# Performance work log

Measured on AMD Instinct MI355X. Metric: run time of the kernel, lower is better.

Reference implementation:

```python
import jax, jax.numpy as jnp
import numpy as np

B, T, C, H = 1, 2048, 1024, 16
K = C // H


def _ln(x, g, b):
    m = x.mean(-1, keepdims=True)
    v = ((x - m) ** 2).mean(-1, keepdims=True)
    return (x - m) * jax.lax.rsqrt(v + 1e-5) * g + b


def setup_inputs() -> dict:
    key = jax.random.key(0)
    ks = jax.random.split(key, 16)
    n = lambda k, s, sc=1.0: jax.random.normal(k, s, jnp.float32) * sc
    u = lambda k, s: jax.random.uniform(k, s, jnp.float32)
    ws = C ** -0.5
    return {
        "x": n(ks[0], (B, T, C)),
        "shift_state": n(ks[1], (B, C)),
        "time_maa_x": u(ks[2], (1, 1, C)),
        "time_maa_r": u(ks[3], (1, 1, C)),
        "time_maa_k": u(ks[4], (1, 1, C)),
        "time_maa_v": u(ks[5], (1, 1, C)),
        "time_maa_w1": n(ks[6], (C, 96), 0.01),
        "time_maa_w2": n(ks[7], (3, 32, C), 0.01),
        "headavg_w1": n(ks[8], (C, 4 * 2 * H), 0.01),
        "headavg_w2": n(ks[9], (4, 2 * H, H), 0.01),
        "w_r": n(ks[10], (C, C), ws),
        "w_k": n(ks[11], (C, C), ws),
        "w_v": n(ks[12], (C, C), ws),
        "w_o": n(ks[13], (C, C), ws),
        "ln_r_g": jnp.ones((C,)), "ln_r_b": jnp.zeros((C,)),
        "ln_k_g": jnp.ones((C,)), "ln_k_b": jnp.zeros((C,)),
        "ln_v_g": jnp.ones((C,)), "ln_v_b": jnp.zeros((C,)),
        "ln_x_g": jnp.ones((C,)), "ln_x_b": jnp.zeros((C,)),
    }


def reference(x, shift_state, time_maa_x, time_maa_r, time_maa_k, time_maa_v,
              time_maa_w1, time_maa_w2, headavg_w1, headavg_w2,
              w_r, w_k, w_v, w_o,
              ln_r_g, ln_r_b, ln_k_g, ln_k_b, ln_v_g, ln_v_b, ln_x_g, ln_x_b):
    Bs, Ts, Cs = x.shape
    Hh = headavg_w2.shape[-1]
    Kk = Cs // Hh

    # token shift
    dxprev = jnp.concatenate([shift_state[:, None, :], x[:, :-1]], axis=1) - x

    # LoRA token-shift mixing
    xxx = jnp.tanh((x + dxprev * time_maa_x) @ time_maa_w1)       # [B,T,3*32]
    mix = jnp.einsum('btnd,ndc->nbtc', xxx.reshape(Bs, Ts, 3, -1), time_maa_w2)
    mq, mk, mv = mix[0], mix[1], mix[2]
    xq = x + dxprev * (time_maa_r + mq)
    xk = x + dxprev * (time_maa_k + mk)
    xv = x + dxprev * (time_maa_v + mv)

    q = _ln(xq @ w_r, ln_r_g, ln_r_b).reshape(Bs, Ts, Hh, Kk).transpose(0, 2, 1, 3)
    k = _ln(xk @ w_k, ln_k_g, ln_k_b).reshape(Bs, Ts, Hh, Kk).transpose(0, 2, 1, 3)
    v = _ln(xv @ w_v, ln_v_g, ln_v_b).reshape(Bs, Ts, Hh, Kk).transpose(0, 2, 1, 3)

    # per-head LoRA score mixing coefficients
    ha = jnp.tanh(x @ headavg_w1).reshape(Bs, Ts, 4, -1)          # [B,T,4,2H]
    hm = jnp.einsum('btnd,ndh->nbth', ha, headavg_w2) / Hh        # [4,B,T,H]
    pre_q, pre_k, post_q, post_k = hm[0], hm[1], hm[2], hm[3]

    scale = Kk ** -0.5
    y = jnp.einsum('bhtk,bhsk->bhts', q * scale, k)               # [B,H,T,S]
    y = y + jnp.einsum('bhts,bth->bts', y, pre_q)[:, None]
    y = y + jnp.einsum('bhts,bsh->bts', y, pre_k)[:, None]

    # causal ALiBi bias
    rel = (jnp.arange(Ts)[:, None] - jnp.arange(Ts)[None, :]).astype(x.dtype)
    slopes = (2.0 ** (-8.0 * jnp.arange(1, Hh + 1, dtype=x.dtype) / Hh))
    bias = jnp.where(rel >= 0, -slopes[:, None, None] * rel, jnp.asarray(-1e9, x.dtype))
    y = y + bias[None]

    y = jax.nn.softmax(y, axis=-1)
    y = y + jnp.einsum('bhts,bth->bts', y, post_q)[:, None]
    y = y + jnp.einsum('bhts,bsh->bts', y, post_k)[:, None]

    out = jnp.einsum('bhts,bhsv->bhtv', y, v).transpose(0, 2, 1, 3).reshape(Bs, Ts, Cs)
    out = _ln(out, ln_x_g, ln_x_b) @ w_o
    return out
```

## Files before the change

### kernel.cpp

```cpp
#include <hip/hip_runtime.h>
#include <cstdint>
#include <cstddef>


#define C_DIM 1024
#define HEADS 16
#define TQ 16
#define SCH 256
#define PADS 40
#define EPS 36

typedef unsigned short ushort_t;
typedef __attribute__((ext_vector_type(8))) short bf16x8;
typedef __attribute__((ext_vector_type(4))) float f32x4;

#define MFMA16(a, b, c) __builtin_amdgcn_mfma_f32_16x16x32_bf16(a, b, c, 0, 0, 0)

__device__ __forceinline__ unsigned int f2bf_u(float f) {
  unsigned int u = __float_as_uint(f);
  return (u + 0x7fffu + ((u >> 16) & 1u)) >> 16;
}
__device__ __forceinline__ float bf2f(ushort_t u) {
  return __uint_as_float(((unsigned int)u) << 16);
}
__device__ __forceinline__ void pack4(ushort_t* dst, float x0, float x1,
                                      float x2, float x3) {
  uint2 v;
  v.x = f2bf_u(x0) | (f2bf_u(x1) << 16);
  v.y = f2bf_u(x2) | (f2bf_u(x3) << 16);
  *(uint2*)dst = v;
}
__device__ __forceinline__ void mlmerge(float& M, float& L, float m2, float l2) {
  float nm = fmaxf(M, m2);
  float ea = (M  <= -1e29f) ? 0.f : __expf(M - nm);
  float eb = (m2 <= -1e29f) ? 0.f : __expf(m2 - nm);
  L = L * ea + l2 * eb;
  M = nm;
}

#define EPHASE(HQARR, HKARR, SSUM) do {                                      \
  if (tid < 128) {                                                           \
    const int tcq = tid >> 3, sq = tid & 7;                                  \
    const int sob = (s1 - sbeg) + sq*4;                                      \
    float a4[4] = {0.f,0.f,0.f,0.f}, b4[4] = {0.f,0.f,0.f,0.f};              \
    _Pragma("unroll")                                                        \
    for (int hq4 = 0; hq4 < 4; hq4++) {                                      \
      float hqa[4];                                                          \
      *(float4*)hqa = *(const float4*)&HQARR[tcq*16 + hq4*4];                \
      float hka[4][4];                                                       \
      _Pragma("unroll")                                                      \
      for (int c = 0; c < 4; c++)                                            \
        *(float4*)hka[c] = *(const float4*)&HKARR[(sob + c)*16 + hq4*4];     \
      _Pragma("unroll")                                                      \
      for (int j = 0; j < 4; j++) {                                          \
        const uint2 yr = *(const uint2*)                                     \
            &ybuf[((hq4*4 + j)*TQ + tcq)*PADS + sq*4];                       \
        float yv[4];                                                         \
        yv[0] = bf2f((ushort_t)(yr.x & 0xffffu));                            \
        yv[1] = bf2f((ushort_t)(yr.x >> 16));                                \
        yv[2] = bf2f((ushort_t)(yr.y & 0xffffu));                            \
        yv[3] = bf2f((ushort_t)(yr.y >> 16));                                \
        _Pragma("unroll")                                                    \
        for (int c = 0; c < 4; c++) {                                        \
          a4[c] += yv[c] * hqa[j];                                           \
          b4[c] += yv[c] * hka[c][j];                                        \
        }                                                                    \
      }                                                                      \
    }                                                                        \
    float ssum[4];                                                           \
    *(float4*)ssum = *(const float4*)&SSUM[sob];                             \
    float4 eo;                                                               \
    eo.x = a4[0]*(1.f + ssum[0]) + b4[0];                                    \
    eo.y = a4[1]*(1.f + ssum[1]) + b4[1];                                    \
    eo.z = a4[2]*(1.f + ssum[2]) + b4[2];                                    \
    eo.w = a4[3]*(1.f + ssum[3]) + b4[3];                                    \
    *(float4*)&ep[tcq*EPS + sq*4] = eo;                                      \
  }                                                                          \
} while (0)

__global__ __launch_bounds__(256) void prep_kernel(
    const float* __restrict__ x, const float* __restrict__ shift,
    const float* __restrict__ maa_x,
    float* __restrict__ dxprev, ushort_t* __restrict__ zbf,
    ushort_t* __restrict__ xbf)
{
  const int t = blockIdx.x;
  const int c = threadIdx.x * 4;
  const size_t base = (size_t)t * C_DIM + c;
  const float4 xc = *(const float4*)&x[base];
  const float4 xp = (t == 0) ? *(const float4*)&shift[c]
                             : *(const float4*)&x[base - C_DIM];
  const float4 mx = *(const float4*)&maa_x[c];
  float4 d;
  d.x = xp.x - xc.x; d.y = xp.y - xc.y; d.z = xp.z - xc.z; d.w = xp.w - xc.w;
  *(float4*)&dxprev[base] = d;
  pack4(&zbf[base], xc.x + d.x*mx.x, xc.y + d.y*mx.y,
        xc.z + d.z*mx.z, xc.w + d.w*mx.w);
  pack4(&xbf[base], xc.x, xc.y, xc.z, xc.w);
}

__global__ __launch_bounds__(256) void wlora_prep(
    const float* __restrict__ w1, const float* __restrict__ hw1,
    ushort_t* __restrict__ wlt)
{
  __shared__ float tile[32][33];
  const int k0 = blockIdx.x*32, j0 = blockIdx.y*32;
  const int r = threadIdx.x >> 3, c4 = (threadIdx.x & 7) * 4;
  const float* W = (j0 < 96) ? w1 : hw1;
  const int stride = (j0 < 96) ? 96 : 128;
  const int jo = (j0 < 96) ? j0 : j0 - 96;
  const float4 v = *(const float4*)&W[(size_t)(k0+r)*stride + jo + c4];
  tile[r][c4+0] = v.x; tile[r][c4+1] = v.y;
  tile[r][c4+2] = v.z; tile[r][c4+3] = v.w;
  __syncthreads();
  pack4(&wlt[(size_t)(j0+r)*C_DIM + k0 + c4],
        tile[c4+0][r], tile[c4+1][r], tile[c4+2][r], tile[c4+3][r]);
}

__global__ __launch_bounds__(64)
__attribute__((amdgpu_waves_per_eu(2, 4)))
void lora_gemm(
    const ushort_t* __restrict__ zbf, const ushort_t* __restrict__ xbf,
    const ushort_t* __restrict__ wlt, float* __restrict__ xxx,
    float* __restrict__ ha)
{
  const int nt = blockIdx.y;
  const int bm = blockIdx.x * 32;
  const ushort_t* A = (nt < 3) ? zbf : xbf;
  const int wrow = nt * 32;
  const int lane = threadIdx.x;
  const int l15 = lane & 15, g = lane >> 4;
  f32x4 acc[2][2];
  #pragma unroll
  for (int i = 0; i < 2; i++)
    #pragma unroll
    for (int j = 0; j < 2; j++) acc[i][j] = (f32x4){0.f,0.f,0.f,0.f};
  bf16x8 a0[2], b0[2], a1[2], b1[2];
  #define LLA(dst, kk) { \
    dst[0] = *(const bf16x8*)&A[(size_t)(bm + l15)*C_DIM + (kk) + g*8]; \
    dst[1] = *(const bf16x8*)&A[(size_t)(bm + 16 + l15)*C_DIM + (kk) + g*8]; }
  #define LLB(dst, kk) { \
    dst[0] = *(const bf16x8*)&wlt[(size_t)(wrow + l15)*C_DIM + (kk) + g*8]; \
    dst[1] = *(const bf16x8*)&wlt[(size_t)(wrow + 16 + l15)*C_DIM + (kk) + g*8]; }
  LLA(a0, 0); LLB(b0, 0);
  for (int k0 = 0; k0 < C_DIM; k0 += 64) {
    LLA(a1, k0+32); LLB(b1, k0+32);
    #pragma unroll
    for (int i = 0; i < 2; i++)
      #pragma unroll
      for (int j = 0; j < 2; j++) acc[i][j] = MFMA16(a0[i], b0[j], acc[i][j]);
    if (k0 + 64 < C_DIM) { LLA(a0, k0+64); LLB(b0, k0+64); }
    #pragma unroll
    for (int i = 0; i < 2; i++)
      #pragma unroll
      for (int j = 0; j < 2; j++) acc[i][j] = MFMA16(a1[i], b1[j], acc[i][j]);
  }
  #undef LLA
  #undef LLB
  #pragma unroll
  for (int i = 0; i < 2; i++)
    #pragma unroll
    for (int j = 0; j < 2; j++)
      #pragma unroll
      for (int r = 0; r < 4; r++) {
        const int t = bm + i*16 + g*4 + r;
        const int col = wrow + j*16 + l15;
        const float val = tanhf(acc[i][j][r]);
        if (nt < 3) xxx[(size_t)t*96 + col] = val;
        else        ha[(size_t)t*128 + col - 96] = val;
      }
}

__global__ __launch_bounds__(256) void mix_kernel(
    const float* __restrict__ x, const float* __restrict__ dxp,
    const float* __restrict__ xxx,
    const float* __restrict__ maa_r, const float* __restrict__ maa_k,
    const float* __restrict__ maa_v, const float* __restrict__ w2,
    ushort_t* __restrict__ xq, ushort_t* __restrict__ xk,
    ushort_t* __restrict__ xv)
{
  __shared__ float xs[8][96];
  const int t0 = blockIdx.x * 8;
  const int tid = threadIdx.x;
  #pragma unroll
  for (int i = 0; i < 3; i++) {
    const int u = tid + i*256;
    if (u < 768) {
      const int r = u / 96, cc = u % 96;
      xs[r][cc] = xxx[(size_t)(t0+r)*96 + cc];
    }
  }
  __syncthreads();
  const int c = tid * 4;
  float4 xc[8], dx[8];
  #pragma unroll
  for (int r = 0; r < 8; r++) {
    xc[r] = *(const float4*)&x[(size_t)(t0+r)*C_DIM + c];
    dx[r] = *(const float4*)&dxp[(size_t)(t0+r)*C_DIM + c];
  }
  const float* maas[3] = {maa_r, maa_k, maa_v};
  ushort_t* outs[3] = {xq, xk, xv};
  #pragma unroll
  for (int n = 0; n < 3; n++) {
    const float4 mv = *(const float4*)&maas[n][c];
    float m[8][4];
    #pragma unroll
    for (int r = 0; r < 8; r++) {
      m[r][0] = mv.x; m[r][1] = mv.y; m[r][2] = mv.z; m[r][3] = mv.w;
    }
    #pragma unroll 8
    for (int d = 0; d < 32; d++) {
      const float4 w = *(const float4*)&w2[((size_t)n*32 + d)*C_DIM + c];
      #pragma unroll
      for (int r = 0; r < 8; r++) {
        const float xv2 = xs[r][n*32 + d];
        m[r][0] += xv2*w.x; m[r][1] += xv2*w.y;
        m[r][2] += xv2*w.z; m[r][3] += xv2*w.w;
      }
    }
    #pragma unroll
    for (int r = 0; r < 8; r++)
      pack4(&outs[n][(size_t)(t0+r)*C_DIM + c],
            xc[r].x + dx[r].x*m[r][0], xc[r].y + dx[r].y*m[r][1],
            xc[r].z + dx[r].z*m[r][2], xc[r].w + dx[r].w*m[r][3]);
  }
}

__global__ __launch_bounds__(256) void hm_kernel(
    const float* __restrict__ ha, const float* __restrict__ hw2,
    float* __restrict__ hm, int T)
{
  const int t = blockIdx.x*4 + (threadIdx.x >> 6);
  const int u = threadIdx.x & 63;
  const int n = u >> 4, h = u & 15;
  float s = 0.f;
  #pragma unroll 8
  for (int d = 0; d < 32; d++)
    s += ha[(size_t)t*128 + n*32 + d] * hw2[(size_t)(n*32 + d)*16 + h];
  hm[((size_t)n*T + t)*16 + h] = s * (1.f/16.f);
}

__global__ __launch_bounds__(256) void wprep_kernel(
    const float* __restrict__ w0, const float* __restrict__ w1,
    const float* __restrict__ w2, const float* __restrict__ w3,
    ushort_t* __restrict__ o0, ushort_t* __restrict__ o1,
    ushort_t* __restrict__ o2, ushort_t* __restrict__ o3)
{
  const float* W; ushort_t* O;
  if (blockIdx.z == 0)      { W = w0; O = o0; }
  else if (blockIdx.z == 1) { W = w1; O = o1; }
  else if (blockIdx.z == 2) { W = w2; O = o2; }
  else                      { W = w3; O = o3; }
  __shared__ float tile[32][33];
  const int k0 = blockIdx.x*32, n0 = blockIdx.y*32;
  const int r = threadIdx.x >> 3, c4 = (threadIdx.x & 7) * 4;
  const float4 v = *(const float4*)&W[(size_t)(k0+r)*C_DIM + n0 + c4];
  tile[r][c4+0] = v.x; tile[r][c4+1] = v.y;
  tile[r][c4+2] = v.z; tile[r][c4+3] = v.w;
  __syncthreads();
  pack4(&O[(size_t)(n0+r)*C_DIM + k0 + c4],
        tile[c4+0][r], tile[c4+1][r], tile[c4+2][r], tile[c4+3][r]);
}

__global__ __launch_bounds__(64)
__attribute__((amdgpu_waves_per_eu(2, 4)))
void gemm_bf16(
    const ushort_t* __restrict__ A, const ushort_t* __restrict__ Bt,
    float* __restrict__ Cm)
{
  const int bid = blockIdx.x;
  const int bn = (bid & 15) * 64;
  const int bm = (bid >> 4) * 32;
  const int lane = threadIdx.x;
  const int l15 = lane & 15, g = lane >> 4;
  f32x4 acc[2][4];
  #pragma unroll
  for (int i = 0; i < 2; i++)
    #pragma unroll
    for (int j = 0; j < 4; j++) acc[i][j] = (f32x4){0.f,0.f,0.f,0.f};
  bf16x8 a0[2], b0[4], a1[2], b1[4];
  #define LGA(dst, kk) { \
    _Pragma("unroll") \
    for (int i = 0; i < 2; i++) \
      dst[i] = *(const bf16x8*)&A[(size_t)(bm + i*16 + l15)*C_DIM + (kk) + g*8]; }
  #define LGB(dst, kk) { \
    _Pragma("unroll") \
    for (int j = 0; j < 4; j++) \
      dst[j] = *(const bf16x8*)&Bt[(size_t)(bn + j*16 + l15)*C_DIM + (kk) + g*8]; }
  LGA(a0, 0); LGB(b0, 0);
  for (int k0 = 0; k0 < C_DIM; k0 += 64) {
    LGA(a1, k0+32); LGB(b1, k0+32);
    #pragma unroll
    for (int i = 0; i < 2; i++)
      #pragma unroll
      for (int j = 0; j < 4; j++) acc[i][j] = MFMA16(a0[i], b0[j], acc[i][j]);
    if (k0 + 64 < C_DIM) { LGA(a0, k0+64); LGB(b0, k0+64); }
    #pragma unroll
    for (int i = 0; i < 2; i++)
      #pragma unroll
      for (int j = 0; j < 4; j++) acc[i][j] = MFMA16(a1[i], b1[j], acc[i][j]);
  }
  #undef LGA
  #undef LGB
  #pragma unroll
  for (int i = 0; i < 2; i++)
    #pragma unroll
    for (int j = 0; j < 4; j++)
      #pragma unroll
      for (int r = 0; r < 4; r++)
        Cm[(size_t)(bm + i*16 + g*4 + r)*C_DIM + bn + j*16 + l15] = acc[i][j][r];
}

__global__ __launch_bounds__(256) void ln_rows(
    const float* __restrict__ in, ushort_t* __restrict__ outp,
    const float* __restrict__ g, const float* __restrict__ b, float scale)
{
  __shared__ float red[4];
  const int t = blockIdx.x;
  const int tid = threadIdx.x;
  const int c = tid*4;
  const float4 v = *(const float4*)&in[(size_t)t*C_DIM + c];
  float s = v.x+v.y+v.z+v.w;
  #pragma unroll
  for (int off = 32; off > 0; off >>= 1) s += __shfl_down(s, off, 64);
  if ((tid & 63) == 0) red[tid >> 6] = s;
  __syncthreads();
  const float mean = (red[0]+red[1]+red[2]+red[3]) * (1.0f/C_DIM);
  __syncthreads();
  const float d0 = v.x-mean, d1 = v.y-mean, d2 = v.z-mean, d3 = v.w-mean;
  float q = d0*d0 + d1*d1 + d2*d2 + d3*d3;
  #pragma unroll
  for (int off = 32; off > 0; off >>= 1) q += __shfl_down(q, off, 64);
  if ((tid & 63) == 0) red[tid >> 6] = q;
  __syncthreads();
  const float var = (red[0]+red[1]+red[2]+red[3]) * (1.0f/C_DIM);
  const float rstd = rsqrtf(var + 1e-5f);
  const float4 gv = *(const float4*)&g[c];
  const float4 bv = *(const float4*)&b[c];
  pack4(outp + (size_t)t*C_DIM + c,
        (d0*rstd*gv.x + bv.x)*scale, (d1*rstd*gv.y + bv.y)*scale,
        (d2*rstd*gv.z + bv.z)*scale, (d3*rstd*gv.w + bv.w)*scale);
}

__global__ __launch_bounds__(256) void vtrans_kernel(
    const ushort_t* __restrict__ vbf, ushort_t* __restrict__ Vt, int T)
{
  __shared__ ushort_t tile[32][36];
  const int t0 = blockIdx.x*32, c0 = blockIdx.y*32;
  const int r = threadIdx.x >> 3, c4 = (threadIdx.x & 7) * 4;
  const uint2 raw = *(const uint2*)&vbf[(size_t)(t0+r)*C_DIM + c0 + c4];
  tile[r][c4+0] = (ushort_t)(raw.x & 0xffffu);
  tile[r][c4+1] = (ushort_t)(raw.x >> 16);
  tile[r][c4+2] = (ushort_t)(raw.y & 0xffffu);
  tile[r][c4+3] = (ushort_t)(raw.y >> 16);
  __syncthreads();
  uint2 w;
  w.x = (unsigned)tile[c4+0][r] | ((unsigned)tile[c4+1][r] << 16);
  w.y = (unsigned)tile[c4+2][r] | ((unsigned)tile[c4+3][r] << 16);
  *(uint2*)&Vt[(size_t)(c0+r)*T + t0 + c4] = w;
}

__global__ __launch_bounds__(512)
__attribute__((amdgpu_waves_per_eu(2, 4)))
void attn_stats(
    const ushort_t* __restrict__ qbf, const ushort_t* __restrict__ kbf,
    const float* __restrict__ hmb, float* __restrict__ part_m,
    float* __restrict__ part_l, int T)
{
  __shared__ ushort_t ybuf[HEADS*TQ*PADS];
  __shared__ float ep[TQ*EPS];
  __shared__ float hpqf[TQ*16];
  __shared__ float hpkf[SCH*16];
  __shared__ float spk_l[SCH];

  const int tbi = (int)blockIdx.y;
  const int tb = (T/TQ) - 1 - tbi;
  const int sc = (tbi & 1) ? (7 - (int)blockIdx.x) : (int)blockIdx.x;
  const int t0 = tb * TQ;
  const int sbeg = sc * SCH;
  if (sbeg >= t0 + TQ) return;
  const int send = (sbeg + SCH < t0 + TQ) ? (sbeg + SCH) : (t0 + TQ);

  const int tid = threadIdx.x;
  const int w = tid >> 6, lane = tid & 63, l15 = lane & 15, g = lane >> 4;

  for (int i = tid; i < SCH*16; i += 512)
    hpkf[i] = hmb[((size_t)1*T + sbeg)*16 + i];
  if (tid < TQ*16)
    hpqf[tid] = hmb[((size_t)0*T + t0)*16 + tid];
  if (tid < SCH) {
    const float* src = hmb + ((size_t)1*T + sbeg + tid)*16;
    float s = 0.f;
    #pragma unroll
    for (int q4 = 0; q4 < 4; q4++) {
      const float4 v = *(const float4*)&src[q4*4];
      s += v.x + v.y + v.z + v.w;
    }
    spk_l[tid] = s;
  }

  const int hh[2] = {w, w + 8};
  bf16x8 qf[2][2];
  float slope[2];
  #pragma unroll
  for (int hd = 0; hd < 2; hd++) {
    #pragma unroll
    for (int kc = 0; kc < 2; kc++)
      qf[hd][kc] = *(const bf16x8*)
          &qbf[(size_t)(t0 + l15)*C_DIM + hh[hd]*64 + kc*32 + g*8];
    slope[hd] = exp2f(-0.5f * (float)(hh[hd] + 1));
  }
  float mrun[2] = {-1e30f, -1e30f}, lrun[2] = {0.f, 0.f};

  bf16x8 kf[2][2][2];
  #define LOADK(sbase) { \
    _Pragma("unroll") \
    for (int hd = 0; hd < 2; hd++) \
      _Pragma("unroll") \
      for (int sh = 0; sh < 2; sh++) \
        _Pragma("unroll") \
        for (int kc = 0; kc < 2; kc++) \
          kf[hd][sh][kc] = *(const bf16x8*)&kbf[ \
              (size_t)((sbase) + sh*16 + l15)*C_DIM + hh[hd]*64 + kc*32 + g*8]; }
  LOADK(sbeg);

  for (int s1 = sbeg; s1 < send; s1 += 32) {
    f32x4 acc[2][2];
    #pragma unroll
    for (int hd = 0; hd < 2; hd++)
      #pragma unroll
      for (int sh = 0; sh < 2; sh++) acc[hd][sh] = (f32x4){0.f,0.f,0.f,0.f};
    #pragma unroll
    for (int hd = 0; hd < 2; hd++) {
      #pragma unroll
      for (int sh = 0; sh < 2; sh++)
        #pragma unroll
        for (int kc = 0; kc < 2; kc++)
          acc[hd][sh] = MFMA16(kf[hd][sh][kc], qf[hd][kc], acc[hd][sh]);
      #pragma unroll
      for (int sh = 0; sh < 2; sh++)
        pack4(&ybuf[(size_t)(hh[hd]*TQ + l15)*PADS + sh*16 + g*4],
              acc[hd][sh][0], acc[hd][sh][1], acc[hd][sh][2], acc[hd][sh][3]);
    }
    {
      const int snx = (s1 + 32 < send) ? s1 + 32 : s1;
      LOADK(snx);
    }
    __syncthreads();
    EPHASE(hpqf, hpkf, spk_l);
    __syncthreads();
    float epv[2][4];
    #pragma unroll
    for (int sh = 0; sh < 2; sh++)
      *(float4*)epv[sh] = *(const float4*)&ep[l15*EPS + sh*16 + g*4];
    #pragma unroll
    for (int hd = 0; hd < 2; hd++) {
      const int t = t0 + l15;
      #pragma unroll
      for (int sh = 0; sh < 2; sh++)
        #pragma unroll
        for (int r = 0; r < 4; r++) {
          const int s = s1 + sh*16 + g*4 + r;
          if (s <= t) {
            const float y3 = acc[hd][sh][r] + epv[sh][r]
                - slope[hd]*(float)(t - s);
            const float d = y3 - mrun[hd];
            if (d > 0.f) { lrun[hd] = lrun[hd]*__expf(-d) + 1.f; mrun[hd] = y3; }
            else lrun[hd] += __expf(d);
          }
        }
    }
  }
  #undef LOADK
  #pragma unroll
  for (int hd = 0; hd < 2; hd++) {
    float M = mrun[hd], L = lrun[hd];
    #pragma unroll
    for (int mask = 16; mask < 64; mask <<= 1) {
      const float M2 = __shfl_xor(M, mask, 64);
      const float L2 = __shfl_xor(L, mask, 64);
      mlmerge(M, L, M2, L2);
    }
    if (g == 0) {
      part_m[(size_t)(sc*HEADS + hh[hd])*T + t0 + l15] = M;
      part_l[(size_t)(sc*HEADS + hh[hd])*T + t0 + l15] = L;
    }
  }
}

__global__ __launch_bounds__(256) void ml_combine(
    const float* __restrict__ part_m, const float* __restrict__ part_l,
    float* __restrict__ m_fin, float* __restrict__ linv, int T)
{
  const int idx = blockIdx.x*256 + threadIdx.x;
  const int t = idx & (T - 1);
  const int nsc = (t >> 8) + 1;
  float M = -1e30f, L = 0.f;
  for (int sc = 0; sc < nsc; sc++)
    mlmerge(M, L, part_m[(size_t)sc*HEADS*T + idx],
            part_l[(size_t)sc*HEADS*T + idx]);
  m_fin[idx] = M;
  linv[idx] = 1.f / L;
}

__global__ __launch_bounds__(512)
__attribute__((amdgpu_waves_per_eu(2, 4)))
void attn_apply(
    const ushort_t* __restrict__ qbf, const ushort_t* __restrict__ kbf,
    const ushort_t* __restrict__ Vt, const float* __restrict__ hmb,
    const float* __restrict__ m_fin, const float* __restrict__ linv,
    float* __restrict__ P, int T)
{
  __shared__ ushort_t ybuf[HEADS*TQ*PADS];
  __shared__ float ep[TQ*EPS];
  __shared__ float hpqf[TQ*16], hoqf[TQ*16];
  __shared__ float hpkf[SCH*16], hokf[SCH*16];
  __shared__ float spk_l[SCH], spo_l[SCH];

  const int tbi = (int)blockIdx.y;
  const int tb = (T/TQ) - 1 - tbi;
  const int sc = (tbi & 1) ? (7 - (int)blockIdx.x) : (int)blockIdx.x;
  const int t0 = tb * TQ;
  const int sbeg = sc * SCH;
  if (sbeg >= t0 + TQ) return;
  const int send = (sbeg + SCH < t0 + TQ) ? (sbeg + SCH) : (t0 + TQ);
  const int prow0 = T*sc - 128*sc*(sc-1) - SCH*sc;

  const int tid = threadIdx.x;
  const int w = tid >> 6, lane = tid & 63, l15 = lane & 15, g = lane >> 4;

  for (int i = tid; i < SCH*16; i += 512) {
    hpkf[i] = hmb[((size_t)1*T + sbeg)*16 + i];
    hokf[i] = hmb[((size_t)3*T + sbeg)*16 + i];
  }
  if (tid < TQ*16) {
    hpqf[tid] = hmb[((size_t)0*T + t0)*16 + tid];
    hoqf[tid] = hmb[((size_t)2*T + t0)*16 + tid];
  }
  {
    const int s_l = tid & 255;
    const float* src = hmb + ((size_t)((tid < 256) ? 1 : 3)*T + sbeg + s_l)*16;
    float s = 0.f;
    #pragma unroll
    for (int q4 = 0; q4 < 4; q4++) {
      const float4 v = *(const float4*)&src[q4*4];
      s += v.x + v.y + v.z + v.w;
    }
    if (tid < 256) spk_l[s_l] = s; else spo_l[s_l] = s;
  }

  const int hh[2] = {w, w + 8};
  bf16x8 qf[2][2];
  float mt[2], li[2], slope[2];
  #pragma unroll
  for (int hd = 0; hd < 2; hd++) {
    #pragma unroll
    for (int kc = 0; kc < 2; kc++)
      qf[hd][kc] = *(const bf16x8*)
          &qbf[(size_t)(t0 + l15)*C_DIM + hh[hd]*64 + kc*32 + g*8];
    mt[hd] = m_fin[(size_t)hh[hd]*T + t0 + l15];
    li[hd] = linv[(size_t)hh[hd]*T + t0 + l15];
    slope[hd] = exp2f(-0.5f * (float)(hh[hd] + 1));
  }
  f32x4 oacc[2][4];
  #pragma unroll
  for (int hd = 0; hd < 2; hd++)
    #pragma unroll
    for (int vf = 0; vf < 4; vf++) oacc[hd][vf] = (f32x4){0.f,0.f,0.f,0.f};

  for (int s1 = sbeg; s1 < send; s1 += 32) {
    f32x4 acc[2][2];
    #pragma unroll
    for (int hd = 0; hd < 2; hd++)
      #pragma unroll
      for (int sh = 0; sh < 2; sh++) acc[hd][sh] = (f32x4){0.f,0.f,0.f,0.f};
    #pragma unroll
    for (int hd = 0; hd < 2; hd++) {
      #pragma unroll
      for (int sh = 0; sh < 2; sh++)
        #pragma unroll
        for (int kc = 0; kc < 2; kc++) {
          const bf16x8 kf = *(const bf16x8*)
              &kbf[(size_t)(s1 + sh*16 + l15)*C_DIM + hh[hd]*64 + kc*32 + g*8];
          acc[hd][sh] = MFMA16(kf, qf[hd][kc], acc[hd][sh]);
        }
      #pragma unroll
      for (int sh = 0; sh < 2; sh++)
        pack4(&ybuf[(size_t)(hh[hd]*TQ + l15)*PADS + sh*16 + g*4],
              acc[hd][sh][0], acc[hd][sh][1], acc[hd][sh][2], acc[hd][sh][3]);
    }
    __syncthreads();
    EPHASE(hpqf, hpkf, spk_l);
    __syncthreads();
    {
      float epv[2][4];
      #pragma unroll
      for (int sh = 0; sh < 2; sh++)
        *(float4*)epv[sh] = *(const float4*)&ep[l15*EPS + sh*16 + g*4];
      #pragma unroll
      for (int hd = 0; hd < 2; hd++) {
        const int t = t0 + l15;
        #pragma unroll
        for (int sh = 0; sh < 2; sh++) {
          #pragma unroll
          for (int r = 0; r < 4; r++) {
            const int s = s1 + sh*16 + g*4 + r;
            float p = 0.f;
            if (s <= t) {
              const float y3 = acc[hd][sh][r] + epv[sh][r]
                  - slope[hd]*(float)(t - s);
              p = __expf(y3 - mt[hd]) * li[hd];
            }
            acc[hd][sh][r] = p;
          }
          pack4(&ybuf[(size_t)(hh[hd]*TQ + l15)*PADS + sh*16 + g*4],
                acc[hd][sh][0], acc[hd][sh][1], acc[hd][sh][2], acc[hd][sh][3]);
        }
      }
    }
    __syncthreads();
    EPHASE(hoqf, hokf, spo_l);
    __syncthreads();
    bf16x8 vv[2][4];
    #pragma unroll
    for (int hd = 0; hd < 2; hd++)
      #pragma unroll
      for (int vf = 0; vf < 4; vf++)
        vv[hd][vf] = *(const bf16x8*)
            &Vt[(size_t)(hh[hd]*64 + vf*16 + l15)*T + s1 + g*8];
    {
      float epv[2][4];
      #pragma unroll
      for (int sh = 0; sh < 2; sh++)
        *(float4*)epv[sh] = *(const float4*)&ep[l15*EPS + sh*16 + g*4];
      #pragma unroll
      for (int hd = 0; hd < 2; hd++)
        #pragma unroll
        for (int sh = 0; sh < 2; sh++)
          pack4(&ybuf[(size_t)(hh[hd]*TQ + l15)*PADS + sh*16 + g*4],
                acc[hd][sh][0] + epv[sh][0], acc[hd][sh][1] + epv[sh][1],
                acc[hd][sh][2] + epv[sh][2], acc[hd][sh][3] + epv[sh][3]);
    }
    #pragma unroll
    for (int hd = 0; hd < 2; hd++) {
      const bf16x8 pa = *(const bf16x8*)
          &ybuf[(size_t)(hh[hd]*TQ + l15)*PADS + g*8];
      #pragma unroll
      for (int vf = 0; vf < 4; vf++)
        oacc[hd][vf] = MFMA16(pa, vv[hd][vf], oacc[hd][vf]);
    }
  }
  #pragma unroll
  for (int hd = 0; hd < 2; hd++)
    #pragma unroll
    for (int vf = 0; vf < 4; vf++)
      #pragma unroll
      for (int r = 0; r < 4; r++)
        P[(size_t)(prow0 + t0 + g*4 + r)*C_DIM + hh[hd]*64 + vf*16 + l15]
            = oacc[hd][vf][r];
}

__global__ __launch_bounds__(256) void reduce_ln(
    const float* __restrict__ P, ushort_t* __restrict__ outp,
    const float* __restrict__ g, const float* __restrict__ b, int T)
{
  __shared__ float red[4];
  const int t = blockIdx.x;
  const int tid = threadIdx.x;
  const int c = tid*4;
  const int nsc = (t >> 8) + 1;
  float4 v = make_float4(0.f, 0.f, 0.f, 0.f);
  int off = 0;
  for (int sc = 0; sc < nsc; sc++) {
    const int row = off + t - sc*SCH;
    const float4 pv = *(const float4*)&P[(size_t)row*C_DIM + c];
    v.x += pv.x; v.y += pv.y; v.z += pv.z; v.w += pv.w;
    off += T - SCH*sc;
  }
  float s = v.x+v.y+v.z+v.w;
  #pragma unroll
  for (int o = 32; o > 0; o >>= 1) s += __shfl_down(s, o, 64);
  if ((tid & 63) == 0) red[tid >> 6] = s;
  __syncthreads();
  const float mean = (red[0]+red[1]+red[2]+red[3]) * (1.0f/C_DIM);
  __syncthreads();
  const float d0 = v.x-mean, d1 = v.y-mean, d2 = v.z-mean, d3 = v.w-mean;
  float q = d0*d0 + d1*d1 + d2*d2 + d3*d3;
  #pragma unroll
  for (int o = 32; o > 0; o >>= 1) q += __shfl_down(q, o, 64);
  if ((tid & 63) == 0) red[tid >> 6] = q;
  __syncthreads();
  const float var = (red[0]+red[1]+red[2]+red[3]) * (1.0f/C_DIM);
  const float rstd = rsqrtf(var + 1e-5f);
  const float4 gv = *(const float4*)&g[c];
  const float4 bv = *(const float4*)&b[c];
  pack4(outp + (size_t)t*C_DIM + c,
        d0*rstd*gv.x + bv.x, d1*rstd*gv.y + bv.y,
        d2*rstd*gv.z + bv.z, d3*rstd*gv.w + bv.w);
}

extern "C" void kernel_launch(void* const* d_in, const int* in_sizes, int n_in,
                              void* d_out, int out_size, void* d_ws, size_t ws_size,
                              hipStream_t stream)
{
  const float* x      = (const float*)d_in[0];
  const float* shift  = (const float*)d_in[1];
  const float* maa_x  = (const float*)d_in[2];
  const float* maa_r  = (const float*)d_in[3];
  const float* maa_k  = (const float*)d_in[4];
  const float* maa_v  = (const float*)d_in[5];
  const float* w1     = (const float*)d_in[6];
  const float* w2     = (const float*)d_in[7];
  const float* hw1    = (const float*)d_in[8];
  const float* hw2    = (const float*)d_in[9];
  const float* w_r    = (const float*)d_in[10];
  const float* w_k    = (const float*)d_in[11];
  const float* w_v    = (const float*)d_in[12];
  const float* w_o    = (const float*)d_in[13];
  const float* ln_r_g = (const float*)d_in[14];
  const float* ln_r_b = (const float*)d_in[15];
  const float* ln_k_g = (const float*)d_in[16];
  const float* ln_k_b = (const float*)d_in[17];
  const float* ln_v_g = (const float*)d_in[18];
  const float* ln_v_b = (const float*)d_in[19];
  const float* ln_x_g = (const float*)d_in[20];
  const float* ln_x_b = (const float*)d_in[21];

  const int T = in_sizes[0] / C_DIM;
  const size_t MM = (size_t)T * C_DIM;
  const size_t HF = MM / 2;

  float* ws = (float*)d_ws;
  float*    P      = ws;
  float*    dxprev = ws;
  ushort_t* zbf    = (ushort_t*)(ws + MM);
  ushort_t* xbf    = (ushort_t*)(ws + MM + HF);
  float*    gtmp   = ws + 2*MM;
  ushort_t* xqb    = (ushort_t*)(ws + 3*MM);
  ushort_t* xkb    = (ushort_t*)(ws + 3*MM + HF);
  ushort_t* xvb    = (ushort_t*)(ws + 4*MM);
  float* base2 = ws + 4*MM + HF;
  ushort_t* qbf = (ushort_t*)(base2 + 0*HF);
  ushort_t* kbf = (ushort_t*)(base2 + 1*HF);
  ushort_t* vbf = (ushort_t*)(base2 + 2*HF);
  ushort_t* Vt  = (ushort_t*)(base2 + 3*HF);
  ushort_t* wtr = (ushort_t*)(base2 + 4*HF);
  ushort_t* wtk = wtr + (size_t)C_DIM*C_DIM;
  ushort_t* wtv = wtk + (size_t)C_DIM*C_DIM;
  ushort_t* wto = wtv + (size_t)C_DIM*C_DIM;
  float* after_w = base2 + 4*HF + (size_t)2*C_DIM*C_DIM;
  ushort_t* wlt = (ushort_t*)after_w;
  float* xxx    = after_w + 131072;
  float* ha     = xxx + (size_t)T*96;
  float* hmb    = ha + (size_t)T*128;
  float* part_m = hmb + (size_t)4*T*16;
  float* part_l = part_m + (size_t)8*HEADS*T;
  float* m_fin  = part_l + (size_t)8*HEADS*T;
  float* linv   = m_fin + (size_t)HEADS*T;
  ushort_t* abf = (ushort_t*)(linv + (size_t)HEADS*T);

  prep_kernel<<<T, 256, 0, stream>>>(x, shift, maa_x, dxprev, zbf, xbf);
  wlora_prep<<<dim3(C_DIM/32, 7), 256, 0, stream>>>(w1, hw1, wlt);
  lora_gemm<<<dim3(T/32, 7), 64, 0, stream>>>(zbf, xbf, wlt, xxx, ha);
  mix_kernel<<<T/8, 256, 0, stream>>>(x, dxprev, xxx, maa_r, maa_k, maa_v, w2,
                                      xqb, xkb, xvb);
  hm_kernel<<<T/4, 256, 0, stream>>>(ha, hw2, hmb, T);
  wprep_kernel<<<dim3(32, 32, 4), 256, 0, stream>>>(
      w_r, w_k, w_v, w_o, wtr, wtk, wtv, wto);

  const int ggemm = (T/32) * (C_DIM/64);
  gemm_bf16<<<ggemm, 64, 0, stream>>>(xqb, wtr, gtmp);
  ln_rows<<<T, 256, 0, stream>>>(gtmp, qbf, ln_r_g, ln_r_b, 0.125f);
  gemm_bf16<<<ggemm, 64, 0, stream>>>(xkb, wtk, gtmp);
  ln_rows<<<T, 256, 0, stream>>>(gtmp, kbf, ln_k_g, ln_k_b, 1.0f);
  gemm_bf16<<<ggemm, 64, 0, stream>>>(xvb, wtv, gtmp);
  ln_rows<<<T, 256, 0, stream>>>(gtmp, vbf, ln_v_g, ln_v_b, 1.0f);
  vtrans_kernel<<<dim3(T/32, C_DIM/32), 256, 0, stream>>>(vbf, Vt, T);

  attn_stats<<<dim3(8, T/TQ), 512, 0, stream>>>(
      qbf, kbf, hmb, part_m, part_l, T);
  ml_combine<<<(HEADS*T)/256, 256, 0, stream>>>(part_m, part_l, m_fin, linv, T);
  attn_apply<<<dim3(8, T/TQ), 512, 0, stream>>>(
      qbf, kbf, Vt, hmb, m_fin, linv, P, T);

  reduce_ln<<<T, 256, 0, stream>>>(P, abf, ln_x_g, ln_x_b, T);
  gemm_bf16<<<ggemm, 64, 0, stream>>>(abf, wto, (float*)d_out);
}
```

Measured before the change: 545.4 us.

## Precompute pre-softmax head-mixing term as a single extended-K GEMM

Folds the pre_q/pre_k cross-head mixing of raw scores into one dense T×T matrix E. E is computed by a new bf16 MFMA GEMM over concatenated [q*pre_q, q] and [k*(1+sum pre_k), k*pre_k] operands. The stats and apply attention kernels then read E from global memory instead of rebuilding it per tile through LDS with two barriers per step. This removes the per-tile EPHASE pass and its synchronisation, at the cost of an extra T×T fp32 buffer write and read, a prep kernel, and bf16 rounding of the scaled operands.

```diff
diff --git a/kernel.cpp b/kernel.cpp
--- a/kernel.cpp
+++ b/kernel.cpp
@@ -360,19 +360,95 @@
   *(uint2*)&Vt[(size_t)(c0+r)*T + t0 + c4] = w;
 }
 
+__global__ __launch_bounds__(256) void qek_prep(
+    const ushort_t* __restrict__ qbf, const ushort_t* __restrict__ kbf,
+    const float* __restrict__ hmb, ushort_t* __restrict__ Qe,
+    ushort_t* __restrict__ Ke, int T)
+{
+  const int t = blockIdx.x;
+  const int tid = threadIdx.x;
+  const int c4 = tid * 4;
+  const int h = tid >> 4;
+  float sp = 0.f;
+  #pragma unroll
+  for (int q4 = 0; q4 < 4; q4++) {
+    const float4 v = *(const float4*)&hmb[((size_t)1*T + t)*16 + q4*4];
+    sp += v.x + v.y + v.z + v.w;
+  }
+  const float preq = hmb[((size_t)0*T + t)*16 + h];
+  const float prek = hmb[((size_t)1*T + t)*16 + h];
+  const uint2 qr = *(const uint2*)&qbf[(size_t)t*C_DIM + c4];
+  const uint2 kr = *(const uint2*)&kbf[(size_t)t*C_DIM + c4];
+  float qv[4], kv[4];
+  qv[0] = bf2f((ushort_t)(qr.x & 0xffffu)); qv[1] = bf2f((ushort_t)(qr.x >> 16));
+  qv[2] = bf2f((ushort_t)(qr.y & 0xffffu)); qv[3] = bf2f((ushort_t)(qr.y >> 16));
+  kv[0] = bf2f((ushort_t)(kr.x & 0xffffu)); kv[1] = bf2f((ushort_t)(kr.x >> 16));
+  kv[2] = bf2f((ushort_t)(kr.y & 0xffffu)); kv[3] = bf2f((ushort_t)(kr.y >> 16));
+  const size_t rb = (size_t)t * 2048;
+  pack4(&Qe[rb + c4], qv[0]*preq, qv[1]*preq, qv[2]*preq, qv[3]*preq);
+  *(uint2*)&Qe[rb + 1024 + c4] = qr;
+  const float osp = 1.f + sp;
+  pack4(&Ke[rb + c4], kv[0]*osp, kv[1]*osp, kv[2]*osp, kv[3]*osp);
+  pack4(&Ke[rb + 1024 + c4], kv[0]*prek, kv[1]*prek, kv[2]*prek, kv[3]*prek);
+}
+
+__global__ __launch_bounds__(64)
+__attribute__((amdgpu_waves_per_eu(2, 4)))
+void e_gemm(
+    const ushort_t* __restrict__ Qe, const ushort_t* __restrict__ Ke,
+    float* __restrict__ E, int T)
+{
+  const int bm = blockIdx.y * 32;
+  const int bn = blockIdx.x * 64;
+  if (bn > bm + 31) return;
+  const int lane = threadIdx.x;
+  const int l15 = lane & 15, g = lane >> 4;
+  const int KD = 2048;
+  f32x4 acc[2][4];
+  #pragma unroll
+  for (int i = 0; i < 2; i++)
+    #pragma unroll
+    for (int j = 0; j < 4; j++) acc[i][j] = (f32x4){0.f,0.f,0.f,0.f};
+  bf16x8 a0[2], b0[4], a1[2], b1[4];
+  #define LEA(dst, kk) { \
+    _Pragma("unroll") \
+    for (int i = 0; i < 2; i++) \
+      dst[i] = *(const bf16x8*)&Qe[(size_t)(bm + i*16 + l15)*KD + (kk) + g*8]; }
+  #define LEB(dst, kk) { \
+    _Pragma("unroll") \
+    for (int j = 0; j < 4; j++) \
+      dst[j] = *(const bf16x8*)&Ke[(size_t)(bn + j*16 + l15)*KD + (kk) + g*8]; }
+  LEA(a0, 0); LEB(b0, 0);
+  for (int k0 = 0; k0 < KD; k0 += 64) {
+    LEA(a1, k0+32); LEB(b1, k0+32);
+    #pragma unroll
+    for (int i = 0; i < 2; i++)
+      #pragma unroll
+      for (int j = 0; j < 4; j++) acc[i][j] = MFMA16(a0[i], b0[j], acc[i][j]);
+    if (k0 + 64 < KD) { LEA(a0, k0+64); LEB(b0, k0+64); }
+    #pragma unroll
+    for (int i = 0; i < 2; i++)
+      #pragma unroll
+      for (int j = 0; j < 4; j++) acc[i][j] = MFMA16(a1[i], b1[j], acc[i][j]);
+  }
+  #undef LEA
+  #undef LEB
+  #pragma unroll
+  for (int i = 0; i < 2; i++)
+    #pragma unroll
+    for (int j = 0; j < 4; j++)
+      #pragma unroll
+      for (int r = 0; r < 4; r++)
+        E[(size_t)(bm + i*16 + g*4 + r)*T + bn + j*16 + l15] = acc[i][j][r];
+}
+
 __global__ __launch_bounds__(512)
 __attribute__((amdgpu_waves_per_eu(2, 4)))
 void attn_stats(
     const ushort_t* __restrict__ qbf, const ushort_t* __restrict__ kbf,
-    const float* __restrict__ hmb, float* __restrict__ part_m,
+    const float* __restrict__ E, float* __restrict__ part_m,
     float* __restrict__ part_l, int T)
 {
-  __shared__ ushort_t ybuf[HEADS*TQ*PADS];
-  __shared__ float ep[TQ*EPS];
-  __shared__ float hpqf[TQ*16];
-  __shared__ float hpkf[SCH*16];
-  __shared__ float spk_l[SCH];
-
   const int tbi = (int)blockIdx.y;
   const int tb = (T/TQ) - 1 - tbi;
   const int sc = (tbi & 1) ? (7 - (int)blockIdx.x) : (int)blockIdx.x;
@@ -383,22 +459,6 @@
 
   const int tid = threadIdx.x;
   const int w = tid >> 6, lane = tid & 63, l15 = lane & 15, g = lane >> 4;
-
-  for (int i = tid; i < SCH*16; i += 512)
-    hpkf[i] = hmb[((size_t)1*T + sbeg)*16 + i];
-  if (tid < TQ*16)
-    hpqf[tid] = hmb[((size_t)0*T + t0)*16 + tid];
-  if (tid < SCH) {
-    const float* src = hmb + ((size_t)1*T + sbeg + tid)*16;
-    float s = 0.f;
-    #pragma unroll
-    for (int q4 = 0; q4 < 4; q4++) {
-      const float4 v = *(const float4*)&src[q4*4];
-      s += v.x + v.y + v.z + v.w;
-    }
-    spk_l[tid] = s;
-  }
-
   const int hh[2] = {w, w + 8};
   bf16x8 qf[2][2];
   float slope[2];
@@ -413,6 +473,7 @@
   float mrun[2] = {-1e30f, -1e30f}, lrun[2] = {0.f, 0.f};
 
   bf16x8 kf[2][2][2];
+  float4 ef[2];
   #define LOADK(sbase) { \
     _Pragma("unroll") \
     for (int hd = 0; hd < 2; hd++) \
@@ -422,7 +483,11 @@
         for (int kc = 0; kc < 2; kc++) \
           kf[hd][sh][kc] = *(const bf16x8*)&kbf[ \
               (size_t)((sbase) + sh*16 + l15)*C_DIM + hh[hd]*64 + kc*32 + g*8]; }
-  LOADK(sbeg);
+  #define LOADE(sbase) { \
+    _Pragma("unroll") \
+    for (int sh = 0; sh < 2; sh++) \
+      ef[sh] = *(const float4*)&E[(size_t)(t0 + l15)*T + (sbase) + sh*16 + g*4]; }
+  LOADK(sbeg); LOADE(sbeg);
 
   for (int s1 = sbeg; s1 < send; s1 += 32) {
     f32x4 acc[2][2];
@@ -431,28 +496,19 @@
       #pragma unroll
       for (int sh = 0; sh < 2; sh++) acc[hd][sh] = (f32x4){0.f,0.f,0.f,0.f};
     #pragma unroll
-    for (int hd = 0; hd < 2; hd++) {
+    for (int hd = 0; hd < 2; hd++)
       #pragma unroll
       for (int sh = 0; sh < 2; sh++)
         #pragma unroll
         for (int kc = 0; kc < 2; kc++)
           acc[hd][sh] = MFMA16(kf[hd][sh][kc], qf[hd][kc], acc[hd][sh]);
-      #pragma unroll
-      for (int sh = 0; sh < 2; sh++)
-        pack4(&ybuf[(size_t)(hh[hd]*TQ + l15)*PADS + sh*16 + g*4],
-              acc[hd][sh][0], acc[hd][sh][1], acc[hd][sh][2], acc[hd][sh][3]);
-    }
+    float efc[2][4];
+    #pragma unroll
+    for (int sh = 0; sh < 2; sh++) *(float4*)efc[sh] = ef[sh];
     {
       const int snx = (s1 + 32 < send) ? s1 + 32 : s1;
-      LOADK(snx);
-    }
-    __syncthreads();
-    EPHASE(hpqf, hpkf, spk_l);
-    __syncthreads();
-    float epv[2][4];
-    #pragma unroll
-    for (int sh = 0; sh < 2; sh++)
-      *(float4*)epv[sh] = *(const float4*)&ep[l15*EPS + sh*16 + g*4];
+      LOADK(snx); LOADE(snx);
+    }
     #pragma unroll
     for (int hd = 0; hd < 2; hd++) {
       const int t = t0 + l15;
@@ -462,7 +518,7 @@
         for (int r = 0; r < 4; r++) {
           const int s = s1 + sh*16 + g*4 + r;
           if (s <= t) {
-            const float y3 = acc[hd][sh][r] + epv[sh][r]
+            const float y3 = acc[hd][sh][r] + efc[sh][r]
                 - slope[hd]*(float)(t - s);
             const float d = y3 - mrun[hd];
             if (d > 0.f) { lrun[hd] = lrun[hd]*__expf(-d) + 1.f; mrun[hd] = y3; }
@@ -472,6 +528,7 @@
     }
   }
   #undef LOADK
+  #undef LOADE
   #pragma unroll
   for (int hd = 0; hd < 2; hd++) {
     float M = mrun[hd], L = lrun[hd];
@@ -507,15 +564,15 @@
 __attribute__((amdgpu_waves_per_eu(2, 4)))
 void attn_apply(
     const ushort_t* __restrict__ qbf, const ushort_t* __restrict__ kbf,
-    const ushort_t* __restrict__ Vt, const float* __restrict__ hmb,
-    const float* __restrict__ m_fin, const float* __restrict__ linv,
-    float* __restrict__ P, int T)
+    const ushort_t* __restrict__ Vt, const float* __restrict__ E,
+    const float* __restrict__ hmb, const float* __restrict__ m_fin,
+    const float* __restrict__ linv, float* __restrict__ P, int T)
 {
   __shared__ ushort_t ybuf[HEADS*TQ*PADS];
   __shared__ float ep[TQ*EPS];
-  __shared__ float hpqf[TQ*16], hoqf[TQ*16];
-  __shared__ float hpkf[SCH*16], hokf[SCH*16];
-  __shared__ float spk_l[SCH], spo_l[SCH];
+  __shared__ float hoqf[TQ*16];
+  __shared__ float hokf[SCH*16];
+  __shared__ float spo_l[SCH];
 
   const int tbi = (int)blockIdx.y;
   const int tb = (T/TQ) - 1 - tbi;
@@ -529,24 +586,19 @@
   const int tid = threadIdx.x;
   const int w = tid >> 6, lane = tid & 63, l15 = lane & 15, g = lane >> 4;
 
-  for (int i = tid; i < SCH*16; i += 512) {
-    hpkf[i] = hmb[((size_t)1*T + sbeg)*16 + i];
+  for (int i = tid; i < SCH*16; i += 512)
     hokf[i] = hmb[((size_t)3*T + sbeg)*16 + i];
-  }
-  if (tid < TQ*16) {
-    hpqf[tid] = hmb[((size_t)0*T + t0)*16 + tid];
+  if (tid < TQ*16)
     hoqf[tid] = hmb[((size_t)2*T + t0)*16 + tid];
-  }
-  {
-    const int s_l = tid & 255;
-    const float* src = hmb + ((size_t)((tid < 256) ? 1 : 3)*T + sbeg + s_l)*16;
+  if (tid < SCH) {
+    const float* src = hmb + ((size_t)3*T + sbeg + tid)*16;
     float s = 0.f;
     #pragma unroll
     for (int q4 = 0; q4 < 4; q4++) {
       const float4 v = *(const float4*)&src[q4*4];
       s += v.x + v.y + v.z + v.w;
     }
-    if (tid < 256) spk_l[s_l] = s; else spo_l[s_l] = s;
+    spo_l[tid] = s;
   }
 
   const int hh[2] = {w, w + 8};
@@ -567,6 +619,7 @@
   for (int hd = 0; hd < 2; hd++)
     #pragma unroll
     for (int vf = 0; vf < 4; vf++) oacc[hd][vf] = (f32x4){0.f,0.f,0.f,0.f};
+  __syncthreads();
 
   for (int s1 = sbeg; s1 < send; s1 += 32) {
     f32x4 acc[2][2];
@@ -574,8 +627,12 @@
     for (int hd = 0; hd < 2; hd++)
       #pragma unroll
       for (int sh = 0; sh < 2; sh++) acc[hd][sh] = (f32x4){0.f,0.f,0.f,0.f};
-    #pragma unroll
-    for (int hd = 0; hd < 2; hd++) {
+    float4 ef[2];
+    #pragma unroll
+    for (int sh = 0; sh < 2; sh++)
+      ef[sh] = *(const float4*)&E[(size_t)(t0 + l15)*T + s1 + sh*16 + g*4];
+    #pragma unroll
+    for (int hd = 0; hd < 2; hd++)
       #pragma unroll
       for (int sh = 0; sh < 2; sh++)
         #pragma unroll
@@ -584,38 +641,24 @@
               &kbf[(size_t)(s1 + sh*16 + l15)*C_DIM + hh[hd]*64 + kc*32 + g*8];
           acc[hd][sh] = MFMA16(kf, qf[hd][kc], acc[hd][sh]);
         }
-      #pragma unroll
-      for (int sh = 0; sh < 2; sh++)
+    #pragma unroll
+    for (int hd = 0; hd < 2; hd++) {
+      const int t = t0 + l15;
+      #pragma unroll
+      for (int sh = 0; sh < 2; sh++) {
+        #pragma unroll
+        for (int r = 0; r < 4; r++) {
+          const int s = s1 + sh*16 + g*4 + r;
+          float p = 0.f;
+          if (s <= t) {
+            const float y3 = acc[hd][sh][r] + ef[sh][r]
+                - slope[hd]*(float)(t - s);
+            p = __expf(y3 - mt[hd]) * li[hd];
+          }
+          acc[hd][sh][r] = p;
+        }
         pack4(&ybuf[(size_t)(hh[hd]*TQ + l15)*PADS + sh*16 + g*4],
               acc[hd][sh][0], acc[hd][sh][1], acc[hd][sh][2], acc[hd][sh][3]);
-    }
-    __syncthreads();
-    EPHASE(hpqf, hpkf, spk_l);
-    __syncthreads();
-    {
-      float epv[2][4];
-      #pragma unroll
-      for (int sh = 0; sh < 2; sh++)
-        *(float4*)epv[sh] = *(const float4*)&ep[l15*EPS + sh*16 + g*4];
-      #pragma unroll
-      for (int hd = 0; hd < 2; hd++) {
-        const int t = t0 + l15;
-        #pragma unroll
-        for (int sh = 0; sh < 2; sh++) {
-          #pragma unroll
-          for (int r = 0; r < 4; r++) {
-            const int s = s1 + sh*16 + g*4 + r;
-            float p = 0.f;
-            if (s <= t) {
-              const float y3 = acc[hd][sh][r] + epv[sh][r]
-                  - slope[hd]*(float)(t - s);
-              p = __expf(y3 - mt[hd]) * li[hd];
-            }
-            acc[hd][sh][r] = p;
-          }
-          pack4(&ybuf[(size_t)(hh[hd]*TQ + l15)*PADS + sh*16 + g*4],
-                acc[hd][sh][0], acc[hd][sh][1], acc[hd][sh][2], acc[hd][sh][3]);
-        }
       }
     }
     __syncthreads();
@@ -739,6 +782,8 @@
   ushort_t* xqb    = (ushort_t*)(ws + 3*MM);
   ushort_t* xkb    = (ushort_t*)(ws + 3*MM + HF);
   ushort_t* xvb    = (ushort_t*)(ws + 4*MM);
+  ushort_t* Qe = (ushort_t*)gtmp;
+  ushort_t* Ke = (ushort_t*)(ws + 3*MM);
   float* base2 = ws + 4*MM + HF;
   ushort_t* qbf = (ushort_t*)(base2 + 0*HF);
   ushort_t* kbf = (ushort_t*)(base2 + 1*HF);
@@ -757,7 +802,9 @@
   float* part_l = part_m + (size_t)8*HEADS*T;
   float* m_fin  = part_l + (size_t)8*HEADS*T;
   float* linv   = m_fin + (size_t)HEADS*T;
-  ushort_t* abf = (ushort_t*)(linv + (size_t)HEADS*T);
+  float* abf_f  = linv + (size_t)HEADS*T;
+  ushort_t* abf = (ushort_t*)abf_f;
+  float* Ebuf   = abf_f + HF;
 
   prep_kernel<<<T, 256, 0, stream>>>(x, shift, maa_x, dxprev, zbf, xbf);
   wlora_prep<<<dim3(C_DIM/32, 7), 256, 0, stream>>>(w1, hw1, wlt);
@@ -777,11 +824,14 @@
   ln_rows<<<T, 256, 0, stream>>>(gtmp, vbf, ln_v_g, ln_v_b, 1.0f);
   vtrans_kernel<<<dim3(T/32, C_DIM/32), 256, 0, stream>>>(vbf, Vt, T);
 
+  qek_prep<<<T, 256, 0, stream>>>(qbf, kbf, hmb, Qe, Ke, T);
+  e_gemm<<<dim3(T/64, T/32), 64, 0, stream>>>(Qe, Ke, Ebuf, T);
+
   attn_stats<<<dim3(8, T/TQ), 512, 0, stream>>>(
-      qbf, kbf, hmb, part_m, part_l, T);
+      qbf, kbf, Ebuf, part_m, part_l, T);
   ml_combine<<<(HEADS*T)/256, 256, 0, stream>>>(part_m, part_l, m_fin, linv, T);
   attn_apply<<<dim3(8, T/TQ), 512, 0, stream>>>(
-      qbf, kbf, Vt, hmb, m_fin, linv, P, T);
+      qbf, kbf, Vt, Ebuf, hmb, m_fin, linv, P, T);
 
   reduce_ln<<<T, 256, 0, stream>>>(P, abf, ln_x_g, ln_x_b, T);
   gemm_bf16<<<ggemm, 64, 0, stream>>>(abf, wto, (float*)d_out);
```

New measurement: 574.6 us. +5.3%, slower.
